# Optimization experiments

Hardware: AMD Instinct MI355X
Metric: run time of the kernel (lower is better)

## Reference

```python
import jax, jax.numpy as jnp
import numpy as np

NUM_HEADS = 16
DIM_HEAD = 64
SCALE = DIM_HEAD ** -0.5
ROPE_BASE = 10000.0


def _rope(t):
    # t: [b, h, n, d] -> rotary embedding with rotate-half convention
    n, d = t.shape[2], t.shape[3]
    inv_freq = 1.0 / (ROPE_BASE ** (jnp.arange(0, d, 2, dtype=jnp.float32) / d))
    freqs = jnp.arange(n, dtype=jnp.float32)[:, None] * inv_freq[None, :]  # [n, d/2]
    cos = jnp.concatenate([jnp.cos(freqs), jnp.cos(freqs)], axis=-1)  # [n, d]
    sin = jnp.concatenate([jnp.sin(freqs), jnp.sin(freqs)], axis=-1)
    t1, t2 = jnp.split(t, 2, axis=-1)
    rot = jnp.concatenate([-t2, t1], axis=-1)
    return t * cos + rot * sin


def setup_inputs() -> dict:
    key = jax.random.key(0)
    k1, k2, k3 = jax.random.split(key, 3)
    B, N, D = 2, 2049, 1024  # 2048 patches + 1 cls token
    x = jax.random.normal(k1, (B, N, D), dtype=jnp.float32)
    ln_gamma = jnp.ones((D,), dtype=jnp.float32)
    ln_beta = jnp.zeros((D,), dtype=jnp.float32)
    w_qkv = jax.random.normal(k2, (D, 3 * NUM_HEADS * DIM_HEAD), dtype=jnp.float32) * 0.02
    w_out = jax.random.normal(k3, (NUM_HEADS * DIM_HEAD, D), dtype=jnp.float32) * 0.02
    return {"x": x, "ln_gamma": ln_gamma, "ln_beta": ln_beta, "w_qkv": w_qkv, "w_out": w_out}


def reference(x, ln_gamma, ln_beta, w_qkv, w_out):
    B, N, D = x.shape
    # LayerNorm (eps=1e-5, torch default)
    mu = jnp.mean(x, axis=-1, keepdims=True)
    var = jnp.mean(jnp.square(x - mu), axis=-1, keepdims=True)
    xn = (x - mu) * jax.lax.rsqrt(var + 1e-5) * ln_gamma + ln_beta
    # QKV projection (no bias)
    qkv = xn @ w_qkv  # [B, N, 3*H*Dh]
    q, k, v = jnp.split(qkv, 3, axis=-1)
    def to_heads(t):
        return t.reshape(B, N, NUM_HEADS, DIM_HEAD).transpose(0, 2, 1, 3)  # [B,H,N,Dh]
    q, k, v = to_heads(q), to_heads(k), to_heads(v)
    # cls token excluded from RoPE
    q = jnp.concatenate([q[:, :, :1, :], _rope(q[:, :, 1:, :])], axis=2)
    k = jnp.concatenate([k[:, :, :1, :], _rope(k[:, :, 1:, :])], axis=2)
    dots = jnp.einsum('bhqd,bhkd->bhqk', q, k) * SCALE
    attn = jax.nn.softmax(dots, axis=-1)
    out = jnp.einsum('bhqk,bhkd->bhqd', attn, v)
    out = out.transpose(0, 2, 1, 3).reshape(B, N, NUM_HEADS * DIM_HEAD)
    return out @ w_out
```

## Files before the change

### kernel.cpp

```cpp
#include <hip/hip_runtime.h>

#define B_    2
#define N_    2049
#define NPAD  2112
#define D_    1024
#define H_    16
#define DH    64
#define MROWS (B_ * N_)
#define MPAD  4224
#define QSCALE 0.18033688011117674f

using bf16x8 = __attribute__((ext_vector_type(8))) short;
using f32x4  = __attribute__((ext_vector_type(4))) float;
using f32x16 = __attribute__((ext_vector_type(16))) float;

#define AS1 __attribute__((address_space(1)))
#define AS3 __attribute__((address_space(3)))

__device__ __forceinline__ float bf2f(short s) {
  union { unsigned u; float f; } a; a.u = ((unsigned)(unsigned short)s) << 16; return a.f;
}
__device__ __forceinline__ short f2bf(float f) {
  union { float f; unsigned u; } a; a.f = f;
  unsigned r = a.u + 0x7fffu + ((a.u >> 16) & 1u);
  return (short)(r >> 16);
}
__device__ __forceinline__ float hexp2(float x) { return __builtin_amdgcn_exp2f(x); }
__device__ __forceinline__ void dma16(const short* g, AS3 short* l) {
  __builtin_amdgcn_global_load_lds((const AS1 unsigned*)g, (AS3 unsigned*)l, 16, 0, 0);
}

__device__ __forceinline__ size_t tiled_off(int m, int k) {
  return ((size_t)(m >> 7) << 17)
       + (size_t)(((k >> 5) << 12)
       + ((((m & 127) >> 4)) << 9)
       + (((((m & 15) << 2) | ((k & 31) >> 3))) << 3)
       + (k & 7));
}

__global__ __launch_bounds__(256) void prep_kernel(const float* __restrict__ x,
                                                   const float* __restrict__ gamma,
                                                   const float* __restrict__ beta,
                                                   short* __restrict__ xn,
                                                   const float* __restrict__ w_qkv,
                                                   short* __restrict__ wqkvT,
                                                   const float* __restrict__ w_out,
                                                   short* __restrict__ woutT) {
  int blk = blockIdx.x;
  int tid = threadIdx.x;
  __shared__ float T[64][65];
  __shared__ float sb[4], s2b[4];

  if (blk < MROWS) {
    int row = blk;
    const float4 v = ((const float4*)(x + (size_t)row * D_))[tid];
    float s  = v.x + v.y + v.z + v.w;
    float ss = v.x * v.x + v.y * v.y + v.z * v.z + v.w * v.w;
    for (int o = 1; o < 64; o <<= 1) { s += __shfl_xor(s, o, 64); ss += __shfl_xor(ss, o, 64); }
    int wid = tid >> 6;
    if ((tid & 63) == 0) { sb[wid] = s; s2b[wid] = ss; }
    __syncthreads();
    float st  = sb[0] + sb[1] + sb[2] + sb[3];
    float sst = s2b[0] + s2b[1] + s2b[2] + s2b[3];
    float mu  = st * (1.0f / D_);
    float var = sst * (1.0f / D_) - mu * mu;
    float rs  = rsqrtf(var + 1e-5f);
    const float4 g  = ((const float4*)gamma)[tid];
    const float4 be = ((const float4*)beta)[tid];
    short4 o4;
    o4.x = f2bf((v.x - mu) * rs * g.x + be.x);
    o4.y = f2bf((v.y - mu) * rs * g.y + be.y);
    o4.z = f2bf((v.z - mu) * rs * g.z + be.z);
    o4.w = f2bf((v.w - mu) * rs * g.w + be.w);
    *(short4*)(xn + tiled_off(row, tid * 4)) = o4;
    return;
  }

  const float* in; short* out; int Nn, t2;
  int b2 = blk - MROWS;
  if (b2 < 768) { in = w_qkv; out = wqkvT; Nn = 3072; t2 = b2; }
  else          { in = w_out; out = woutT; Nn = 1024; t2 = b2 - 768; }
  int k0 = (t2 & 15) * 64;
  int n0 = (t2 >> 4) * 64;
  int r = tid >> 2, c0 = (tid & 3) * 16;
  const float* ip = in + (size_t)(k0 + r) * Nn + n0 + c0;
  #pragma unroll
  for (int j = 0; j < 4; ++j) {
    float4 v = *(const float4*)(ip + j * 4);
    T[r][c0 + j * 4 + 0] = v.x; T[r][c0 + j * 4 + 1] = v.y;
    T[r][c0 + j * 4 + 2] = v.z; T[r][c0 + j * 4 + 3] = v.w;
  }
  __syncthreads();
  bf16x8 w0, w1;
  #pragma unroll
  for (int j = 0; j < 8; ++j) {
    w0[j] = f2bf(T[c0 + j][r]);
    w1[j] = f2bf(T[c0 + 8 + j][r]);
  }
  *(bf16x8*)(out + tiled_off(n0 + r, k0 + c0))     = w0;
  *(bf16x8*)(out + tiled_off(n0 + r, k0 + c0 + 8)) = w1;
}

#define BM 128
#define BK 32
template <typename OutT>
__global__ __launch_bounds__(256) void gemm128(const short* __restrict__ A,
                                               const short* __restrict__ BT,
                                               OutT* __restrict__ C,
                                               int Mstore, int Ncols, int K) {
  int lane = threadIdx.x & 63, wid = threadIdx.x >> 6;
  int quad = lane >> 4, l16 = lane & 15;
  int wr = wid >> 1, wc = wid & 1;
  int chunk = gridDim.x >> 3;
  int swz = (blockIdx.x & 7) * chunk + (blockIdx.x >> 3);
  int mb = swz % 33, nb = swz / 33;
  int m0 = mb * BM;
  int n0 = nb * BM;

  __shared__ __align__(16) short Abuf[2][BM * BK];
  __shared__ __align__(16) short Bbuf[2][BM * BK];
  AS3 short* AbufL = (AS3 short*)&Abuf[0][0];
  AS3 short* BbufL = (AS3 short*)&Bbuf[0][0];

  f32x4 acc[4][4] = {};

  const short* Ap = A  + ((size_t)(m0 >> 7) << 17);
  const short* Bp = BT + ((size_t)(n0 >> 7) << 17);

  auto stage = [&](int kt, int bb) {
    #pragma unroll
    for (int i = 0; i < 2; ++i) {
      int j = wid * 2 + i;
      dma16(Ap + ((size_t)kt << 12) + j * 512 + lane * 8, AbufL + bb * (BM * BK) + j * 512);
      dma16(Bp + ((size_t)kt << 12) + j * 512 + lane * 8, BbufL + bb * (BM * BK) + j * 512);
    }
  };

  stage(0, 0);
  __syncthreads();

  int KT = K / BK;
  for (int kt = 0; kt < KT; ++kt) {
    int cur = kt & 1;
    if (kt + 1 < KT) stage(kt + 1, cur ^ 1);
    const short* Ab = &Abuf[cur][0];
    const short* Bb = &Bbuf[cur][0];
    bf16x8 af[4], bfr[4];
    #pragma unroll
    for (int s = 0; s < 4; ++s)
      af[s] = *(const bf16x8*)&Ab[(wr * 64 + s * 16 + l16) * BK + quad * 8];
    #pragma unroll
    for (int t = 0; t < 4; ++t)
      bfr[t] = *(const bf16x8*)&Bb[(wc * 64 + t * 16 + l16) * BK + quad * 8];
    #pragma unroll
    for (int s = 0; s < 4; ++s)
      #pragma unroll
      for (int t = 0; t < 4; ++t)
        acc[s][t] = __builtin_amdgcn_mfma_f32_16x16x32_bf16(af[s], bfr[t], acc[s][t], 0, 0, 0);
    __syncthreads();
  }

  #pragma unroll
  for (int s = 0; s < 4; ++s)
    #pragma unroll
    for (int r = 0; r < 4; ++r) {
      int row = m0 + wr * 64 + s * 16 + quad * 4 + r;
      if (row < Mstore) {
        size_t rb = (size_t)row * Ncols + n0 + wc * 64;
        #pragma unroll
        for (int t = 0; t < 4; ++t) {
          float val = acc[s][t][r];
          if constexpr (sizeof(OutT) == 2)
            C[rb + t * 16 + l16] = (OutT)(unsigned short)f2bf(val);
          else
            C[rb + t * 16 + l16] = (OutT)val;
        }
      }
    }
}

__global__ __launch_bounds__(256) void rope_kernel(const short* __restrict__ qkv,
                                                   short* __restrict__ qg,
                                                   short* __restrict__ kfrag,
                                                   short* __restrict__ vfrag) {
  int bh = blockIdx.y;
  int n0 = blockIdx.x * 64;
  int b = bh >> 4, h = bh & 15;
  int t = threadIdx.x;
  int nl = t >> 2;
  int p  = t & 3;
  int n  = n0 + nl;
  size_t hb = (size_t)bh * NPAD * DH;
  size_t ob = hb + (size_t)n * DH;

  __shared__ short Vt[64][66];
  __shared__ short Kt[64][66];

  bf16x8 oq1 = {}, oq2 = {}, ok1 = {}, ok2 = {};
  short v1s[8] = {}, v2s[8] = {};
  if (n < N_) {
    size_t ib = ((size_t)(b * N_ + n)) * 3072 + h * DH;
    bf16x8 q1v = *(const bf16x8*)(qkv + ib + p * 8);
    bf16x8 q2v = *(const bf16x8*)(qkv + ib + 32 + p * 8);
    bf16x8 k1v = *(const bf16x8*)(qkv + ib + 1024 + p * 8);
    bf16x8 k2v = *(const bf16x8*)(qkv + ib + 1024 + 32 + p * 8);
    bf16x8 v1v = *(const bf16x8*)(qkv + ib + 2048 + p * 8);
    bf16x8 v2v = *(const bf16x8*)(qkv + ib + 2048 + 32 + p * 8);
    #pragma unroll
    for (int j = 0; j < 8; ++j) {
      int i = p * 8 + j;
      float q1 = bf2f(q1v[j]), q2 = bf2f(q2v[j]);
      float k1 = bf2f(k1v[j]), k2 = bf2f(k2v[j]);
      if (n > 0) {
        float ang = (float)(n - 1) * hexp2((float)i * -0.4152410118609203f);
        float rev = ang * 0.15915494309189535f;
        rev = rev - floorf(rev);
        float sn = __builtin_amdgcn_sinf(rev);
        float cs = __builtin_amdgcn_cosf(rev);
        float nq1 = q1 * cs - q2 * sn, nq2 = q2 * cs + q1 * sn;
        float nk1 = k1 * cs - k2 * sn, nk2 = k2 * cs + k1 * sn;
        q1 = nq1; q2 = nq2; k1 = nk1; k2 = nk2;
      }
      oq1[j] = f2bf(q1 * QSCALE); oq2[j] = f2bf(q2 * QSCALE);
      ok1[j] = f2bf(k1); ok2[j] = f2bf(k2);
      v1s[j] = v1v[j]; v2s[j] = v2v[j];
    }
  }
  *(bf16x8*)(qg + ob + p * 8)      = oq1;
  *(bf16x8*)(qg + ob + 32 + p * 8) = oq2;
  #pragma unroll
  for (int j = 0; j < 8; ++j) {
    Vt[nl][p * 8 + j]      = v1s[j];
    Vt[nl][32 + p * 8 + j] = v2s[j];
    Kt[nl][p * 8 + j]      = ok1[j];
    Kt[nl][32 + p * 8 + j] = ok2[j];
  }
  __syncthreads();

  int l = t & 63, c = t >> 6;
  int lk = l & 31, hi = l >> 5;
  size_t tb = hb + (size_t)(n0 >> 6) * 4096;
  bf16x8 wv0, wv1, wk0, wk1;
  #pragma unroll
  for (int i = 0; i < 8; ++i) {
    int keyr = c * 16 + hi * 8 + i;
    wv0[i] = Vt[keyr][lk];
    wv1[i] = Vt[keyr][32 + lk];
    wk0[i] = Kt[lk][keyr];
    wk1[i] = Kt[32 + lk][keyr];
  }
  *(bf16x8*)(vfrag + tb + (size_t)(0 * 4 + c) * 512 + l * 8) = wv0;
  *(bf16x8*)(vfrag + tb + (size_t)(4 + c) * 512 + l * 8)     = wv1;
  *(bf16x8*)(kfrag + tb + (size_t)(0 * 4 + c) * 512 + l * 8) = wk0;
  *(bf16x8*)(kfrag + tb + (size_t)(4 + c) * 512 + l * 8)     = wk1;
}

__global__ __launch_bounds__(256, 3) void attn_kernel(const short* __restrict__ qg,
                                                      const short* __restrict__ kfrag,
                                                      const short* __restrict__ vfrag,
                                                      short* __restrict__ out) {
  int blk = blockIdx.x;
  int xcd = blk & 7;
  int t_  = blk >> 3;
  int bh  = xcd * 4 + (t_ & 3);
  int qblk = t_ >> 2;
  int b = bh >> 4, h = bh & 15;

  int lane = threadIdx.x & 63, wid = threadIdx.x >> 6;
  int q    = lane & 31;
  int half = lane >> 5;
  int q0   = qblk * 128 + wid * 32;
  size_t hb = (size_t)bh * NPAD * DH;
  const short* kf_hb = kfrag + hb;
  const short* vf_hb = vfrag + hb;

  __shared__ __align__(16) short Kbuf[3][4096];
  __shared__ __align__(16) short Vbuf[3][4096];
  AS3 short* KbufL = (AS3 short*)&Kbuf[0][0];
  AS3 short* VbufL = (AS3 short*)&Vbuf[0][0];
  const short* KbufR = &Kbuf[0][0];
  const short* VbufR = &Vbuf[0][0];

  int qr = q0 + q; if (qr >= NPAD) qr = 0;
  const short* qp = qg + hb + (size_t)qr * DH + half * 8;
  bf16x8 qf[4];
  #pragma unroll
  for (int s = 0; s < 4; ++s) qf[s] = *(const bf16x8*)(qp + s * 16);

  f32x16 o0 = {}, o1 = {};
  float lrun = 0.0f;

  auto stage = [&](int kt, int bb) {
    const short* ksrc = kf_hb + (size_t)kt * 4096;
    const short* vsrc = vf_hb + (size_t)kt * 4096;
    #pragma unroll
    for (int i = 0; i < 2; ++i) {
      int j = wid * 2 + i;
      dma16(ksrc + j * 512 + lane * 8, KbufL + bb * 4096 + j * 512);
      dma16(vsrc + j * 512 + lane * 8, VbufL + bb * 4096 + j * 512);
    }
  };

  stage(0, 0);
  stage(1, 1);

  #define NKT 33
  for (int kt = 0; kt < NKT; ++kt) {
    int rb = kt % 3;
    int k0 = kt * 64;

    if (kt == NKT - 1) asm volatile("s_waitcnt vmcnt(0)" ::: "memory");
    else               asm volatile("s_waitcnt vmcnt(4)" ::: "memory");
    __builtin_amdgcn_s_barrier();

    if (kt + 2 < NKT) stage(kt + 2, (kt + 2) % 3);
    __builtin_amdgcn_sched_barrier(0);

    const short* Vc = VbufR + rb * 4096;
    bf16x8 vf0[4], vf1[4];
    #pragma unroll
    for (int s = 0; s < 4; ++s) {
      vf0[s] = *(const bf16x8*)&Vc[(0 * 4 + s) * 512 + lane * 8];
      vf1[s] = *(const bf16x8*)&Vc[(4 + s) * 512 + lane * 8];
    }

    const short* Kc = KbufR + rb * 4096;
    f32x16 sA = {}, sB = {};
    __builtin_amdgcn_s_setprio(1);
    #pragma unroll
    for (int s = 0; s < 4; ++s) {
      bf16x8 kf0 = *(const bf16x8*)&Kc[(0 * 4 + s) * 512 + lane * 8];
      bf16x8 kf1 = *(const bf16x8*)&Kc[(1 * 4 + s) * 512 + lane * 8];
      sA = __builtin_amdgcn_mfma_f32_32x32x16_bf16(kf0, qf[s], sA, 0, 0, 0);
      sB = __builtin_amdgcn_mfma_f32_32x32x16_bf16(kf1, qf[s], sB, 0, 0, 0);
    }
    __builtin_amdgcn_s_setprio(0);

    if (k0 + 64 > N_) {
      #pragma unroll
      for (int rr = 0; rr < 16; ++rr) {
        int key = (rr & 3) + 8 * (rr >> 2) + 4 * half;
        if (k0 + key >= N_)      sA[rr] = -1e30f;
        if (k0 + 32 + key >= N_) sB[rr] = -1e30f;
      }
    }

    float vsum = 0.0f;
    #pragma unroll
    for (int rr = 0; rr < 16; ++rr) {
      sA[rr] = hexp2(sA[rr]); vsum += sA[rr];
      sB[rr] = hexp2(sB[rr]); vsum += sB[rr];
    }
    lrun += vsum;

    unsigned w[4][4];
    #pragma unroll
    for (int g = 0; g < 2; ++g) {
      #pragma unroll
      for (int fs = 0; fs < 2; ++fs) {
        int b0 = fs * 8;
        float e0, e1, e2, e3, e4, e5, e6, e7;
        if (g == 0) {
          e0 = sA[b0+0]; e1 = sA[b0+1]; e2 = sA[b0+2]; e3 = sA[b0+3];
          e4 = sA[b0+4]; e5 = sA[b0+5]; e6 = sA[b0+6]; e7 = sA[b0+7];
        } else {
          e0 = sB[b0+0]; e1 = sB[b0+1]; e2 = sB[b0+2]; e3 = sB[b0+3];
          e4 = sB[b0+4]; e5 = sB[b0+5]; e6 = sB[b0+6]; e7 = sB[b0+7];
        }
        unsigned X1, X2, Y1, Y2;
        asm("v_cvt_pk_bf16_f32 %0, %1, %2" : "=v"(X1) : "v"(e0), "v"(e1));
        asm("v_cvt_pk_bf16_f32 %0, %1, %2" : "=v"(X2) : "v"(e2), "v"(e3));
        asm("v_cvt_pk_bf16_f32 %0, %1, %2" : "=v"(Y1) : "v"(e4), "v"(e5));
        asm("v_cvt_pk_bf16_f32 %0, %1, %2" : "=v"(Y2) : "v"(e6), "v"(e7));
        asm("v_permlane32_swap_b32 %0, %1" : "+v"(X1), "+v"(Y1));
        asm("v_permlane32_swap_b32 %0, %1" : "+v"(X2), "+v"(Y2));
        int kst = g * 2 + fs;
        w[kst][0] = X1; w[kst][1] = X2; w[kst][2] = Y1; w[kst][3] = Y2;
      }
    }

    __builtin_amdgcn_s_setprio(1);
    #pragma unroll
    for (int kst = 0; kst < 4; ++kst) {
      union { unsigned u[4]; bf16x8 v; } bw;
      bw.u[0] = w[kst][0]; bw.u[1] = w[kst][1]; bw.u[2] = w[kst][2]; bw.u[3] = w[kst][3];
      o0 = __builtin_amdgcn_mfma_f32_32x32x16_bf16(vf0[kst], bw.v, o0, 0, 0, 0);
      o1 = __builtin_amdgcn_mfma_f32_32x32x16_bf16(vf1[kst], bw.v, o1, 0, 0, 0);
    }
    __builtin_amdgcn_s_setprio(0);
  }

  lrun += __shfl_xor(lrun, 32, 64);

  int qrow = q0 + q;
  if (qrow < N_) {
    float inv = 1.0f / lrun;
    int grow = b * N_ + qrow;
    #pragma unroll
    for (int m = 0; m < 2; ++m) {
      #pragma unroll
      for (int gq = 0; gq < 4; ++gq) {
        float a0 = (m ? o1[gq*4+0] : o0[gq*4+0]) * inv;
        float a1 = (m ? o1[gq*4+1] : o0[gq*4+1]) * inv;
        float a2 = (m ? o1[gq*4+2] : o0[gq*4+2]) * inv;
        float a3 = (m ? o1[gq*4+3] : o0[gq*4+3]) * inv;
        short4 st;
        st.x = f2bf(a0); st.y = f2bf(a1); st.z = f2bf(a2); st.w = f2bf(a3);
        int dh = m * 32 + gq * 8 + half * 4;
        *(short4*)(out + tiled_off(grow, h * DH + dh)) = st;
      }
    }
  }
}

extern "C" void kernel_launch(void* const* d_in, const int* in_sizes, int n_in,
                              void* d_out, int out_size, void* d_ws, size_t ws_size,
                              hipStream_t stream) {
  const float* x     = (const float*)d_in[0];
  const float* gamma = (const float*)d_in[1];
  const float* beta  = (const float*)d_in[2];
  const float* w_qkv = (const float*)d_in[3];
  const float* w_out = (const float*)d_in[4];

  short* wqkvT = (short*)d_ws;
  short* woutT = wqkvT + (size_t)3072 * 1024;
  short* xn    = woutT + (size_t)1024 * 1024;
  short* qkv   = xn    + (size_t)MPAD * 1024;
  short* qg    = qkv   + (size_t)MPAD * 3072;
  short* kfragG = qg    + (size_t)B_ * H_ * NPAD * DH;
  short* vfragG = kfragG + (size_t)B_ * H_ * NPAD * DH;
  short* attn_out = xn;

  prep_kernel<<<MROWS + 768 + 256, 256, 0, stream>>>(x, gamma, beta, xn,
                                                     w_qkv, wqkvT, w_out, woutT);
  gemm128<unsigned short><<<792, 256, 0, stream>>>(xn, wqkvT, (unsigned short*)qkv, MROWS, 3072, 1024);
  {
    dim3 g(33, 32);
    rope_kernel<<<g, 256, 0, stream>>>(qkv, qg, kfragG, vfragG);
  }
  attn_kernel<<<544, 256, 0, stream>>>(qg, kfragG, vfragG, attn_out);
  gemm128<float><<<264, 256, 0, stream>>>(attn_out, woutT, (float*)d_out, MROWS, 1024, 1024);
}
```

Before: 220.9 us.

## Fuse RoPE and K/V fragment packing into QKV GEMM epilogue

The QKV projection GEMM now stages its output tile in shared memory. Its epilogue applies RoPE and the Q scale, then writes Q, K-fragment and V-fragment layouts directly, chosen by which third of the output columns the tile covers. This removes the separate rope kernel and the full bf16 qkv intermediate, along with that buffer's global write and re-read. To make M tiles line up with per-batch padded sequence positions, the LayerNorm output now uses a padded row layout. The cost is extra shared-memory traffic and more epilogue work per GEMM block, and the padding rows between batches stay uninitialised but are masked on output.

After: 209.9 us (median of 2 runs). -5.0%, faster.

```diff
diff --git a/kernel.cpp b/kernel.cpp
--- a/kernel.cpp
+++ b/kernel.cpp
@@ -53,6 +53,8 @@
 
   if (blk < MROWS) {
     int row = blk;
+    int b = row >= N_;
+    int rowp = b * NPAD + (row - b * N_);
     const float4 v = ((const float4*)(x + (size_t)row * D_))[tid];
     float s  = v.x + v.y + v.z + v.w;
     float ss = v.x * v.x + v.y * v.y + v.z * v.z + v.w * v.w;
@@ -72,7 +74,7 @@
     o4.y = f2bf((v.y - mu) * rs * g.y + be.y);
     o4.z = f2bf((v.z - mu) * rs * g.z + be.z);
     o4.w = f2bf((v.w - mu) * rs * g.w + be.w);
-    *(short4*)(xn + tiled_off(row, tid * 4)) = o4;
+    *(short4*)(xn + tiled_off(rowp, tid * 4)) = o4;
     return;
   }
 
@@ -103,6 +105,185 @@
 
 #define BM 128
 #define BK 32
+__global__ __launch_bounds__(256) void gemm_qkv_rope(const short* __restrict__ A,
+                                                     const short* __restrict__ BT,
+                                                     short* __restrict__ qg,
+                                                     short* __restrict__ kfrag,
+                                                     short* __restrict__ vfrag) {
+  int lane = threadIdx.x & 63, wid = threadIdx.x >> 6;
+  int quad = lane >> 4, l16 = lane & 15;
+  int wr = wid >> 1, wc = wid & 1;
+  int chunk = gridDim.x >> 3;
+  int swz = (blockIdx.x & 7) * chunk + (blockIdx.x >> 3);
+  int mb = swz % 33, nb = swz / 33;
+  int m0 = mb * BM;
+  int n0 = nb * BM;
+
+  __shared__ __align__(16) short pool[17408];
+  AS3 short* AbufL = (AS3 short*)pool;
+  AS3 short* BbufL = (AS3 short*)(pool + 8192);
+  const short* AbufR = pool;
+  const short* BbufR = pool + 8192;
+
+  f32x4 acc[4][4] = {};
+
+  const short* Ap = A  + ((size_t)(m0 >> 7) << 17);
+  const short* Bp = BT + ((size_t)(n0 >> 7) << 17);
+
+  auto stage = [&](int kt, int bb) {
+    #pragma unroll
+    for (int i = 0; i < 2; ++i) {
+      int j = wid * 2 + i;
+      dma16(Ap + ((size_t)kt << 12) + j * 512 + lane * 8, AbufL + bb * 4096 + j * 512);
+      dma16(Bp + ((size_t)kt << 12) + j * 512 + lane * 8, BbufL + bb * 4096 + j * 512);
+    }
+  };
+
+  stage(0, 0);
+  __syncthreads();
+
+  for (int kt = 0; kt < 32; ++kt) {
+    int cur = kt & 1;
+    if (kt + 1 < 32) stage(kt + 1, cur ^ 1);
+    const short* Ab = AbufR + cur * 4096;
+    const short* Bb = BbufR + cur * 4096;
+    bf16x8 af[4], bfr[4];
+    #pragma unroll
+    for (int s = 0; s < 4; ++s)
+      af[s] = *(const bf16x8*)&Ab[(wr * 64 + s * 16 + l16) * BK + quad * 8];
+    #pragma unroll
+    for (int t = 0; t < 4; ++t)
+      bfr[t] = *(const bf16x8*)&Bb[(wc * 64 + t * 16 + l16) * BK + quad * 8];
+    #pragma unroll
+    for (int s = 0; s < 4; ++s)
+      #pragma unroll
+      for (int t = 0; t < 4; ++t)
+        acc[s][t] = __builtin_amdgcn_mfma_f32_16x16x32_bf16(af[s], bfr[t], acc[s][t], 0, 0, 0);
+    __syncthreads();
+  }
+
+  short* Ct = pool;
+  #pragma unroll
+  for (int s = 0; s < 4; ++s)
+    #pragma unroll
+    for (int t = 0; t < 4; ++t) {
+      int col = wc * 64 + t * 16 + l16;
+      #pragma unroll
+      for (int r = 0; r < 4; ++r) {
+        int row = wr * 64 + s * 16 + quad * 4 + r;
+        Ct[row * 136 + col] = f2bf(acc[s][t][r]);
+      }
+    }
+  __syncthreads();
+
+  int third = nb >> 3;
+  int hpair = (nb & 7) * 2;
+  int tid = threadIdx.x;
+
+  if (third == 0) {
+    int p = tid & 3, nl = tid >> 2;
+    #pragma unroll
+    for (int tt = 0; tt < 2; ++tt) {
+      int rl = tt * 64 + nl;
+      int rg = m0 + rl;
+      int b = rg >= NPAD;
+      int n = rg - b * NPAD;
+      bool valid = n < N_;
+      bool rot = valid && n > 0;
+      float csv[8], snv[8];
+      #pragma unroll
+      for (int j = 0; j < 8; ++j) {
+        int i = p * 8 + j;
+        float ang = rot ? (float)(n - 1) * hexp2((float)i * -0.4152410118609203f) : 0.0f;
+        float rev = ang * 0.15915494309189535f;
+        rev = rev - floorf(rev);
+        snv[j] = rot ? __builtin_amdgcn_sinf(rev) : 0.0f;
+        csv[j] = rot ? __builtin_amdgcn_cosf(rev) : 1.0f;
+      }
+      #pragma unroll
+      for (int hh = 0; hh < 2; ++hh) {
+        bf16x8 w1v = {}, w2v = {};
+        if (valid) {
+          bf16x8 va = *(const bf16x8*)&Ct[rl * 136 + hh * 64 + p * 8];
+          bf16x8 vb = *(const bf16x8*)&Ct[rl * 136 + hh * 64 + p * 8 + 32];
+          #pragma unroll
+          for (int j = 0; j < 8; ++j) {
+            float a = bf2f(va[j]), b2 = bf2f(vb[j]);
+            w1v[j] = f2bf((a * csv[j] - b2 * snv[j]) * QSCALE);
+            w2v[j] = f2bf((b2 * csv[j] + a * snv[j]) * QSCALE);
+          }
+        }
+        size_t ob = ((size_t)(b * 16 + hpair + hh) * NPAD + n) * DH;
+        *(bf16x8*)(qg + ob + p * 8)      = w1v;
+        *(bf16x8*)(qg + ob + 32 + p * 8) = w2v;
+      }
+    }
+  } else if (third == 1) {
+    int rl = tid & 127, hi = tid >> 7;
+    int rg = m0 + rl;
+    int b = rg >= NPAD;
+    int n = rg - b * NPAD;
+    bool valid = n < N_;
+    bool rot = valid && n > 0;
+    int kt = n >> 6, g = (n >> 5) & 1, lk = n & 31;
+    int l = hi * 32 + lk;
+    #pragma unroll
+    for (int s2 = 0; s2 < 2; ++s2) {
+      float csv[8], snv[8];
+      #pragma unroll
+      for (int j = 0; j < 8; ++j) {
+        int i = s2 * 16 + hi * 8 + j;
+        float ang = rot ? (float)(n - 1) * hexp2((float)i * -0.4152410118609203f) : 0.0f;
+        float rev = ang * 0.15915494309189535f;
+        rev = rev - floorf(rev);
+        snv[j] = rot ? __builtin_amdgcn_sinf(rev) : 0.0f;
+        csv[j] = rot ? __builtin_amdgcn_cosf(rev) : 1.0f;
+      }
+      #pragma unroll
+      for (int hh = 0; hh < 2; ++hh) {
+        bf16x8 wlo = {}, whi = {};
+        if (valid) {
+          bf16x8 va = *(const bf16x8*)&Ct[rl * 136 + hh * 64 + s2 * 16 + hi * 8];
+          bf16x8 vb = *(const bf16x8*)&Ct[rl * 136 + hh * 64 + s2 * 16 + hi * 8 + 32];
+          #pragma unroll
+          for (int j = 0; j < 8; ++j) {
+            float a = bf2f(va[j]), b2 = bf2f(vb[j]);
+            wlo[j] = f2bf(a * csv[j] - b2 * snv[j]);
+            whi[j] = f2bf(b2 * csv[j] + a * snv[j]);
+          }
+        }
+        short* base = kfrag + (size_t)(b * 16 + hpair + hh) * NPAD * DH + (size_t)kt * 4096;
+        *(bf16x8*)(base + (g * 4 + s2) * 512 + l * 8)     = wlo;
+        *(bf16x8*)(base + (g * 4 + s2 + 2) * 512 + l * 8) = whi;
+      }
+    }
+  } else {
+    int lk = tid & 31, z = tid >> 5;
+    #pragma unroll
+    for (int oo = 0; oo < 2; ++oo) {
+      int o = z * 2 + oo;
+      int rg = m0 + o * 8;
+      int b = rg >= NPAD;
+      int n0o = rg - b * NPAD;
+      int kt = n0o >> 6;
+      int s = (n0o >> 4) & 3;
+      int hi = (n0o >> 3) & 1;
+      #pragma unroll
+      for (int hh = 0; hh < 2; ++hh) {
+        short* base = vfrag + (size_t)(b * 16 + hpair + hh) * NPAD * DH + (size_t)kt * 4096;
+        #pragma unroll
+        for (int m = 0; m < 2; ++m) {
+          bf16x8 wv = {};
+          #pragma unroll
+          for (int j = 0; j < 8; ++j)
+            if (n0o + j < N_) wv[j] = Ct[(o * 8 + j) * 136 + hh * 64 + m * 32 + lk];
+          *(bf16x8*)(base + (m * 4 + s) * 512 + (hi * 32 + lk) * 8) = wv;
+        }
+      }
+    }
+  }
+}
+
 template <typename OutT>
 __global__ __launch_bounds__(256) void gemm128(const short* __restrict__ A,
                                                const short* __restrict__ BT,
@@ -177,82 +358,6 @@
         }
       }
     }
-}
-
-__global__ __launch_bounds__(256) void rope_kernel(const short* __restrict__ qkv,
-                                                   short* __restrict__ qg,
-                                                   short* __restrict__ kfrag,
-                                                   short* __restrict__ vfrag) {
-  int bh = blockIdx.y;
-  int n0 = blockIdx.x * 64;
-  int b = bh >> 4, h = bh & 15;
-  int t = threadIdx.x;
-  int nl = t >> 2;
-  int p  = t & 3;
-  int n  = n0 + nl;
-  size_t hb = (size_t)bh * NPAD * DH;
-  size_t ob = hb + (size_t)n * DH;
-
-  __shared__ short Vt[64][66];
-  __shared__ short Kt[64][66];
-
-  bf16x8 oq1 = {}, oq2 = {}, ok1 = {}, ok2 = {};
-  short v1s[8] = {}, v2s[8] = {};
-  if (n < N_) {
-    size_t ib = ((size_t)(b * N_ + n)) * 3072 + h * DH;
-    bf16x8 q1v = *(const bf16x8*)(qkv + ib + p * 8);
-    bf16x8 q2v = *(const bf16x8*)(qkv + ib + 32 + p * 8);
-    bf16x8 k1v = *(const bf16x8*)(qkv + ib + 1024 + p * 8);
-    bf16x8 k2v = *(const bf16x8*)(qkv + ib + 1024 + 32 + p * 8);
-    bf16x8 v1v = *(const bf16x8*)(qkv + ib + 2048 + p * 8);
-    bf16x8 v2v = *(const bf16x8*)(qkv + ib + 2048 + 32 + p * 8);
-    #pragma unroll
-    for (int j = 0; j < 8; ++j) {
-      int i = p * 8 + j;
-      float q1 = bf2f(q1v[j]), q2 = bf2f(q2v[j]);
-      float k1 = bf2f(k1v[j]), k2 = bf2f(k2v[j]);
-      if (n > 0) {
-        float ang = (float)(n - 1) * hexp2((float)i * -0.4152410118609203f);
-        float rev = ang * 0.15915494309189535f;
-        rev = rev - floorf(rev);
-        float sn = __builtin_amdgcn_sinf(rev);
-        float cs = __builtin_amdgcn_cosf(rev);
-        float nq1 = q1 * cs - q2 * sn, nq2 = q2 * cs + q1 * sn;
-        float nk1 = k1 * cs - k2 * sn, nk2 = k2 * cs + k1 * sn;
-        q1 = nq1; q2 = nq2; k1 = nk1; k2 = nk2;
-      }
-      oq1[j] = f2bf(q1 * QSCALE); oq2[j] = f2bf(q2 * QSCALE);
-      ok1[j] = f2bf(k1); ok2[j] = f2bf(k2);
-      v1s[j] = v1v[j]; v2s[j] = v2v[j];
-    }
-  }
-  *(bf16x8*)(qg + ob + p * 8)      = oq1;
-  *(bf16x8*)(qg + ob + 32 + p * 8) = oq2;
-  #pragma unroll
-  for (int j = 0; j < 8; ++j) {
-    Vt[nl][p * 8 + j]      = v1s[j];
-    Vt[nl][32 + p * 8 + j] = v2s[j];
-    Kt[nl][p * 8 + j]      = ok1[j];
-    Kt[nl][32 + p * 8 + j] = ok2[j];
-  }
-  __syncthreads();
-
-  int l = t & 63, c = t >> 6;
-  int lk = l & 31, hi = l >> 5;
-  size_t tb = hb + (size_t)(n0 >> 6) * 4096;
-  bf16x8 wv0, wv1, wk0, wk1;
-  #pragma unroll
-  for (int i = 0; i < 8; ++i) {
-    int keyr = c * 16 + hi * 8 + i;
-    wv0[i] = Vt[keyr][lk];
-    wv1[i] = Vt[keyr][32 + lk];
-    wk0[i] = Kt[lk][keyr];
-    wk1[i] = Kt[32 + lk][keyr];
-  }
-  *(bf16x8*)(vfrag + tb + (size_t)(0 * 4 + c) * 512 + l * 8) = wv0;
-  *(bf16x8*)(vfrag + tb + (size_t)(4 + c) * 512 + l * 8)     = wv1;
-  *(bf16x8*)(kfrag + tb + (size_t)(0 * 4 + c) * 512 + l * 8) = wk0;
-  *(bf16x8*)(kfrag + tb + (size_t)(4 + c) * 512 + l * 8)     = wk1;
 }
 
 __global__ __launch_bounds__(256, 3) void attn_kernel(const short* __restrict__ qg,
@@ -425,19 +530,14 @@
   short* wqkvT = (short*)d_ws;
   short* woutT = wqkvT + (size_t)3072 * 1024;
   short* xn    = woutT + (size_t)1024 * 1024;
-  short* qkv   = xn    + (size_t)MPAD * 1024;
-  short* qg    = qkv   + (size_t)MPAD * 3072;
+  short* qg    = xn    + (size_t)MPAD * 1024;
   short* kfragG = qg    + (size_t)B_ * H_ * NPAD * DH;
   short* vfragG = kfragG + (size_t)B_ * H_ * NPAD * DH;
   short* attn_out = xn;
 
   prep_kernel<<<MROWS + 768 + 256, 256, 0, stream>>>(x, gamma, beta, xn,
                                                      w_qkv, wqkvT, w_out, woutT);
-  gemm128<unsigned short><<<792, 256, 0, stream>>>(xn, wqkvT, (unsigned short*)qkv, MROWS, 3072, 1024);
-  {
-    dim3 g(33, 32);
-    rope_kernel<<<g, 256, 0, stream>>>(qkv, qg, kfragG, vfragG);
-  }
+  gemm_qkv_rope<<<792, 256, 0, stream>>>(xn, wqkvT, qg, kfragG, vfragG);
   attn_kernel<<<544, 256, 0, stream>>>(qg, kfragG, vfragG, attn_out);
   gemm128<float><<<264, 256, 0, stream>>>(attn_out, woutT, (float*)d_out, MROWS, 1024, 1024);
 }
```
